# Kernel tuning notes

Hardware: AMD Instinct MI355X
Metric: run time of the kernel (lower is better)

Reference implementation:

```python
import jax, jax.numpy as jnp
import numpy as np

N = 50000      # nodes
E = 800000     # edges (before self-loops)
F_IN = 128     # input node features
H = 4          # attention heads
C = 32         # hidden channels per head (concat width = H*C = 128)
CLS = 40       # num classes (layer 4, concat=False -> mean over heads)
NEG_SLOPE = 0.2


def setup_inputs() -> dict:
    key = jax.random.key(0)
    ks = jax.random.split(key, 16)
    w = lambda k, shape: (jax.random.normal(k, shape, jnp.float32) * 0.1)
    return {
        "x": jax.random.normal(ks[0], (N, F_IN), jnp.float32),
        "edge_index": jax.random.randint(ks[1], (2, E), 0, N),
        "W1": w(ks[2], (F_IN, H * C)), "att_src1": w(ks[3], (H, C)), "att_dst1": w(ks[4], (H, C)), "b1": jnp.zeros((H * C,), jnp.float32),
        "W2": w(ks[5], (H * C, H * C)), "att_src2": w(ks[6], (H, C)), "att_dst2": w(ks[7], (H, C)), "b2": jnp.zeros((H * C,), jnp.float32),
        "W3": w(ks[8], (H * C, H * C)), "att_src3": w(ks[9], (H, C)), "att_dst3": w(ks[10], (H, C)), "b3": jnp.zeros((H * C,), jnp.float32),
        "W4": w(ks[11], (H * C, H * CLS)), "att_src4": w(ks[12], (H, CLS)), "att_dst4": w(ks[13], (H, CLS)), "b4": jnp.zeros((CLS,), jnp.float32),
    }


def _gat(x, W, a_src, a_dst, b, src, dst, n, heads, ch, concat):
    # Linear transform, per-head view: [n, heads, ch]
    h = (x @ W).reshape(n, heads, ch)
    # per-node scalar attention terms [n, heads]
    es = (h * a_src).sum(-1)
    ed = (h * a_dst).sum(-1)
    # edge logits: alpha_j (source) + alpha_i (target), leaky relu (PyG GATConv)
    e = jax.nn.leaky_relu(es[src] + ed[dst], NEG_SLOPE)  # [Etot, heads]
    # segment softmax over incoming edges of each dst node (self-loops guarantee >=1 edge)
    m = jax.ops.segment_max(e, dst, num_segments=n)
    ealpha = jnp.exp(e - m[dst])
    denom = jax.ops.segment_sum(ealpha, dst, num_segments=n)
    alpha = ealpha / denom[dst]
    # weighted message aggregation (scatter-add)
    out = jax.ops.segment_sum(h[src] * alpha[:, :, None], dst, num_segments=n)
    out = out.reshape(n, heads * ch) if concat else out.mean(axis=1)
    return out + b


def reference(x, edge_index, W1, att_src1, att_dst1, b1, W2, att_src2, att_dst2, b2,
              W3, att_src3, att_dst3, b3, W4, att_src4, att_dst4, b4):
    n = x.shape[0]
    loop = jnp.arange(n)
    src = jnp.concatenate([edge_index[0], loop])  # add self-loops (PyG default)
    dst = jnp.concatenate([edge_index[1], loop])
    # dropout layers are identity in eval mode (training=False)
    h = _gat(x, W1, att_src1, att_dst1, b1, src, dst, n, H, C, True)
    h = jax.nn.relu(h)
    h = _gat(h, W2, att_src2, att_dst2, b2, src, dst, n, H, C, True)
    h = jax.nn.relu(h)
    h = _gat(h, W3, att_src3, att_dst3, b3, src, dst, n, H, C, True)
    h = jax.nn.relu(h)
    h = _gat(h, W4, att_src4, att_dst4, b4, src, dst, n, H, CLS, False)
    return h
```

## Files before the change

### kernel.cpp

```cpp
#include <hip/hip_runtime.h>
#include <math.h>

#define NN 50000
#define EE 800000
#define ET (EE + NN)
#define NCHK ((NN + 255) / 256)
#define NEG 0.2f

__device__ __forceinline__ float lrelu(float x) { return x > 0.f ? x : NEG * x; }

typedef __bf16 bf16x8 __attribute__((ext_vector_type(8)));
typedef float f32x4 __attribute__((ext_vector_type(4)));


__global__ __launch_bounds__(256) void k_hist(const int* __restrict__ eidx, int* __restrict__ cnt) {
    int i = blockIdx.x * 256 + threadIdx.x;
    if (i < EE) atomicAdd(&cnt[eidx[EE + i]], 1);
}

__global__ __launch_bounds__(256) void k_csum(const int* __restrict__ cnt, int* __restrict__ csums) {
    __shared__ int sh[256];
    int t = threadIdx.x, i = blockIdx.x * 256 + t;
    sh[t] = (i < NN) ? cnt[i] + 1 : 0;
    __syncthreads();
    for (int off = 128; off > 0; off >>= 1) {
        if (t < off) sh[t] += sh[t + off];
        __syncthreads();
    }
    if (t == 0) csums[blockIdx.x] = sh[0];
}

__global__ __launch_bounds__(256) void k_chscan(const int* __restrict__ cnt, const int* __restrict__ csums,
                                                int* __restrict__ rowptr, int* __restrict__ cursor) {
    __shared__ int sh[256];
    __shared__ int shc[256];
    int t = threadIdx.x, b = blockIdx.x, i = b * 256 + t;
    int v = (i < NN) ? cnt[i] + 1 : 0;
    sh[t] = v;
    shc[t] = (t < NCHK) ? csums[t] : 0;
    __syncthreads();
    for (int off = 1; off < 256; off <<= 1) {
        int x1 = (t >= off) ? sh[t - off] : 0;
        int x2 = (t >= off) ? shc[t - off] : 0;
        __syncthreads();
        sh[t] += x1;
        shc[t] += x2;
        __syncthreads();
    }
    int cbase = (b == 0) ? 0 : shc[b - 1];
    int ex = (t == 0 ? 0 : sh[t - 1]) + cbase;
    if (i < NN) { rowptr[i] = ex; cursor[i] = ex; }
    if (b == 0 && t == 0) rowptr[NN] = ET;
}

__global__ __launch_bounds__(256) void k_scatter(const int* __restrict__ eidx,
                                                 int* __restrict__ cursor, int* __restrict__ ssrc) {
    int i = blockIdx.x * 256 + threadIdx.x;
    if (i >= ET) return;
    int s, d;
    if (i < EE) { s = eidx[i]; d = eidx[EE + i]; } else { s = d = i - EE; }
    int pos = atomicAdd(&cursor[d], 1);
    ssrc[pos] = s;
}


__global__ __launch_bounds__(256) void k_wsplit_all(const float* __restrict__ W0, const float* __restrict__ W1,
                                                    const float* __restrict__ W2, const float* __restrict__ W3,
                                                    __bf16* __restrict__ wsp) {
    int i = blockIdx.x * 256 + threadIdx.x;
    const float* Wm; int NOUT, j; size_t base, sz;
    if (i < 16384)      { Wm = W0; NOUT = 128; j = i;          base = 0;     sz = 16384; }
    else if (i < 32768) { Wm = W1; NOUT = 128; j = i - 16384;  base = 32768; sz = 16384; }
    else if (i < 49152) { Wm = W2; NOUT = 128; j = i - 32768;  base = 65536; sz = 16384; }
    else if (i < 69632) { Wm = W3; NOUT = 160; j = i - 49152;  base = 98304; sz = 20480; }
    else return;
    float v = Wm[j];
    int k = j / NOUT, c = j - k * NOUT;
    __bf16 hi = (__bf16)v;
    __bf16 lo = (__bf16)(v - (float)hi);
    size_t off = base + ((size_t)(k >> 3) * NOUT + c) * 8 + (k & 7);
    wsp[off] = hi;
    wsp[off + sz] = lo;
}


template <int NOUT, bool FUSE>
__global__ __launch_bounds__(256) void k_gemm3(const float* __restrict__ X,
                                               const __bf16* __restrict__ Whi,
                                               const __bf16* __restrict__ Wlo,
                                               float* __restrict__ Y,
                                               const float* __restrict__ asrc,
                                               const float* __restrict__ adst,
                                               float* __restrict__ es, float* __restrict__ ed) {
    constexpr int NT = NOUT / 16;
    constexpr int CH = NOUT / 4;
    int tid = threadIdx.x;
    int w = tid >> 6, l = tid & 63;
    int col = l & 15, kg = l >> 4;
    int rb = blockIdx.x * 128 + w * 32;
    int r0 = rb + col, r1 = rb + 16 + col;
    int rc0 = r0 < NN ? r0 : NN - 1;
    int rc1 = r1 < NN ? r1 : NN - 1;

    f32x4 acc0[NT], acc1[NT];
    #pragma unroll
    for (int t = 0; t < NT; ++t) { acc0[t] = (f32x4){0,0,0,0}; acc1[t] = (f32x4){0,0,0,0}; }

    #pragma unroll
    for (int c4 = 0; c4 < 4; ++c4) {
        bf16x8 ah0, al0, ah1, al1;
        {
            float4 aA = *reinterpret_cast<const float4*>(&X[(size_t)rc0 * 128 + c4 * 32 + kg * 8]);
            float4 aB = *reinterpret_cast<const float4*>(&X[(size_t)rc0 * 128 + c4 * 32 + kg * 8 + 4]);
            float av[8] = {aA.x, aA.y, aA.z, aA.w, aB.x, aB.y, aB.z, aB.w};
            #pragma unroll
            for (int j = 0; j < 8; ++j) { __bf16 h = (__bf16)av[j]; ah0[j] = h; al0[j] = (__bf16)(av[j] - (float)h); }
        }
        {
            float4 aA = *reinterpret_cast<const float4*>(&X[(size_t)rc1 * 128 + c4 * 32 + kg * 8]);
            float4 aB = *reinterpret_cast<const float4*>(&X[(size_t)rc1 * 128 + c4 * 32 + kg * 8 + 4]);
            float av[8] = {aA.x, aA.y, aA.z, aA.w, aB.x, aB.y, aB.z, aB.w};
            #pragma unroll
            for (int j = 0; j < 8; ++j) { __bf16 h = (__bf16)av[j]; ah1[j] = h; al1[j] = (__bf16)(av[j] - (float)h); }
        }
        const __bf16* bh = Whi + ((size_t)(c4 * 4 + kg) * NOUT) * 8;
        const __bf16* bl = Wlo + ((size_t)(c4 * 4 + kg) * NOUT) * 8;
        #pragma unroll
        for (int t = 0; t < NT; ++t) {
            bf16x8 bhi = *reinterpret_cast<const bf16x8*>(bh + (t * 16 + col) * 8);
            bf16x8 blo = *reinterpret_cast<const bf16x8*>(bl + (t * 16 + col) * 8);
            acc0[t] = __builtin_amdgcn_mfma_f32_16x16x32_bf16(ah0, bhi, acc0[t], 0, 0, 0);
            acc0[t] = __builtin_amdgcn_mfma_f32_16x16x32_bf16(al0, bhi, acc0[t], 0, 0, 0);
            acc0[t] = __builtin_amdgcn_mfma_f32_16x16x32_bf16(ah0, blo, acc0[t], 0, 0, 0);
            acc1[t] = __builtin_amdgcn_mfma_f32_16x16x32_bf16(ah1, bhi, acc1[t], 0, 0, 0);
            acc1[t] = __builtin_amdgcn_mfma_f32_16x16x32_bf16(al1, bhi, acc1[t], 0, 0, 0);
            acc1[t] = __builtin_amdgcn_mfma_f32_16x16x32_bf16(ah1, blo, acc1[t], 0, 0, 0);
        }
    }

    #pragma unroll
    for (int t = 0; t < NT; ++t) {
        int cc = t * 16 + col;
        #pragma unroll
        for (int i = 0; i < 4; ++i) {
            int ra = rb + kg * 4 + i;
            int rbq = rb + 16 + kg * 4 + i;
            if (ra < NN)  Y[(size_t)ra  * NOUT + cc] = acc0[t][i];
            if (rbq < NN) Y[(size_t)rbq * NOUT + cc] = acc1[t][i];
        }
    }

    if constexpr (FUSE) {
        float pes[2][4][4], ped[2][4][4];
        #pragma unroll
        for (int rt = 0; rt < 2; ++rt)
            #pragma unroll
            for (int h = 0; h < 4; ++h)
                #pragma unroll
                for (int i = 0; i < 4; ++i) { pes[rt][h][i] = 0.f; ped[rt][h][i] = 0.f; }
        #pragma unroll
        for (int t = 0; t < NT; ++t) {
            float as = asrc[t * 16 + col];
            float ad = adst[t * 16 + col];
            int hA = (t * 16) / CH;
            int hB = (t * 16 + 15) / CH;
            if (hA == hB) {
                #pragma unroll
                for (int i = 0; i < 4; ++i) {
                    pes[0][hA][i] += acc0[t][i] * as;  ped[0][hA][i] += acc0[t][i] * ad;
                    pes[1][hA][i] += acc1[t][i] * as;  ped[1][hA][i] += acc1[t][i] * ad;
                }
            } else {
                bool isB = (col >= (hB * CH - t * 16));
                #pragma unroll
                for (int i = 0; i < 4; ++i) {
                    float vs0 = acc0[t][i] * as, vd0 = acc0[t][i] * ad;
                    float vs1 = acc1[t][i] * as, vd1 = acc1[t][i] * ad;
                    pes[0][hA][i] += isB ? 0.f : vs0;  pes[0][hB][i] += isB ? vs0 : 0.f;
                    ped[0][hA][i] += isB ? 0.f : vd0;  ped[0][hB][i] += isB ? vd0 : 0.f;
                    pes[1][hA][i] += isB ? 0.f : vs1;  pes[1][hB][i] += isB ? vs1 : 0.f;
                    ped[1][hA][i] += isB ? 0.f : vd1;  ped[1][hB][i] += isB ? vd1 : 0.f;
                }
            }
        }
        #pragma unroll
        for (int off = 1; off < 16; off <<= 1) {
            #pragma unroll
            for (int rt = 0; rt < 2; ++rt)
                #pragma unroll
                for (int h = 0; h < 4; ++h)
                    #pragma unroll
                    for (int i = 0; i < 4; ++i) {
                        pes[rt][h][i] += __shfl_xor(pes[rt][h][i], off);
                        ped[rt][h][i] += __shfl_xor(ped[rt][h][i], off);
                    }
        }
        if (col == 0) {
            #pragma unroll
            for (int rt = 0; rt < 2; ++rt)
                #pragma unroll
                for (int i = 0; i < 4; ++i) {
                    int rr = rb + rt * 16 + kg * 4 + i;
                    if (rr < NN) {
                        #pragma unroll
                        for (int h = 0; h < 4; ++h) {
                            es[rr * 4 + h] = pes[rt][h][i];
                            ed[rr * 4 + h] = ped[rt][h][i];
                        }
                    }
                }
        }
    }
}


__global__ __launch_bounds__(256) void k_agg128(const float* __restrict__ Hf,
                                                const float* __restrict__ es, const float* __restrict__ ed,
                                                const int* __restrict__ rowptr, const int* __restrict__ ssrc,
                                                const float* __restrict__ bias, float* __restrict__ Yout) {
    int wid = (blockIdx.x * 256 + threadIdx.x) >> 6;
    int lane = threadIdx.x & 63;
    if (wid >= NN) return;
    int n = wid;
    int beg = rowptr[n], end = rowptr[n + 1];
    int h1 = lane & 3;
    int eoff = lane >> 2;
    float edv = ed[n * 4 + h1];

    float m = -1e30f, dsum = 0.f;
    for (int idx = beg + eoff; idx < end; idx += 16) {
        int s = ssrc[idx];
        float e = lrelu(es[s * 4 + h1] + edv);
        float M = fmaxf(m, e);
        dsum = dsum * __expf(m - M) + __expf(e - M);
        m = M;
    }
    #pragma unroll
    for (int off = 4; off < 64; off <<= 1) {
        float om = __shfl_xor(m, off);
        float od = __shfl_xor(dsum, off);
        float M = fmaxf(m, om);
        dsum = dsum * __expf(m - M) + od * __expf(om - M);
        m = M;
    }
    float invd = 1.f / dsum;

    int q = lane & 7;
    int eg8 = lane >> 3;
    f32x4 acc4[4];
    #pragma unroll
    for (int i = 0; i < 4; ++i) acc4[i] = (f32x4){0.f, 0.f, 0.f, 0.f};

    int nch = (end - beg + 15) >> 4;
    int base = beg;
    for (int ch = 0; ch < nch; ++ch, base += 16) {
        int myIdx = base + eoff;
        int s = ssrc[myIdx < end ? myIdx : end - 1];
        float e = lrelu(es[s * 4 + h1] + edv);
        float alpha = (myIdx < end) ? __expf(e - m) * invd : 0.f;
        #pragma unroll
        for (int hb = 0; hb < 2; ++hb) {
            int e16 = hb * 8 + eg8;
            int se = __shfl(s, e16 * 4);
            const float* rowp = Hf + (size_t)se * 128 + q * 4;
            #pragma unroll
            for (int i = 0; i < 4; ++i) {
                float p = __shfl(alpha, e16 * 4 + i);
                float4 v = *reinterpret_cast<const float4*>(rowp + i * 32);
                acc4[i].x += p * v.x;
                acc4[i].y += p * v.y;
                acc4[i].z += p * v.z;
                acc4[i].w += p * v.w;
            }
        }
    }

    #pragma unroll
    for (int off = 8; off < 64; off <<= 1) {
        #pragma unroll
        for (int i = 0; i < 4; ++i) {
            acc4[i].x += __shfl_xor(acc4[i].x, off);
            acc4[i].y += __shfl_xor(acc4[i].y, off);
            acc4[i].z += __shfl_xor(acc4[i].z, off);
            acc4[i].w += __shfl_xor(acc4[i].w, off);
        }
    }
    if (lane < 8) {
        #pragma unroll
        for (int i = 0; i < 4; ++i) {
            int c0 = 32 * i + 4 * lane;
            float4 bv = *reinterpret_cast<const float4*>(&bias[c0]);
            float4 o;
            o.x = fmaxf(acc4[i].x + bv.x, 0.f);
            o.y = fmaxf(acc4[i].y + bv.y, 0.f);
            o.z = fmaxf(acc4[i].z + bv.z, 0.f);
            o.w = fmaxf(acc4[i].w + bv.w, 0.f);
            *reinterpret_cast<float4*>(&Yout[(size_t)n * 128 + c0]) = o;
        }
    }
}


__global__ __launch_bounds__(256) void k_agg160_mean(const float* __restrict__ Hf,
                                                     const float* __restrict__ es, const float* __restrict__ ed,
                                                     const int* __restrict__ rowptr, const int* __restrict__ ssrc,
                                                     const float* __restrict__ b4, float* __restrict__ out) {
    __shared__ float buf[4][160];
    int wid = (blockIdx.x * 256 + threadIdx.x) >> 6;
    int lane = threadIdx.x & 63;
    int w = threadIdx.x >> 6;
    if (wid >= NN) return;
    int n = wid;
    int beg = rowptr[n], end = rowptr[n + 1];
    int h1 = lane & 3;
    int eoff = lane >> 2;
    float edv = ed[n * 4 + h1];

    float m = -1e30f, dsum = 0.f;
    for (int idx = beg + eoff; idx < end; idx += 16) {
        int s = ssrc[idx];
        float e = lrelu(es[s * 4 + h1] + edv);
        float M = fmaxf(m, e);
        dsum = dsum * __expf(m - M) + __expf(e - M);
        m = M;
    }
    #pragma unroll
    for (int off = 4; off < 64; off <<= 1) {
        float om = __shfl_xor(m, off);
        float od = __shfl_xor(dsum, off);
        float M = fmaxf(m, om);
        dsum = dsum * __expf(m - M) + od * __expf(om - M);
        m = M;
    }
    float invd = 1.f / dsum;

    int q = lane & 7;
    int eg8 = lane >> 3;
    int hh[5];
    #pragma unroll
    for (int i = 0; i < 5; ++i) hh[i] = (i * 8 + q) / 10;
    f32x4 acc4[5];
    #pragma unroll
    for (int i = 0; i < 5; ++i) acc4[i] = (f32x4){0.f, 0.f, 0.f, 0.f};

    int nch = (end - beg + 15) >> 4;
    int base = beg;
    for (int ch = 0; ch < nch; ++ch, base += 16) {
        int myIdx = base + eoff;
        int s = ssrc[myIdx < end ? myIdx : end - 1];
        float e = lrelu(es[s * 4 + h1] + edv);
        float alpha = (myIdx < end) ? __expf(e - m) * invd : 0.f;
        #pragma unroll
        for (int hb = 0; hb < 2; ++hb) {
            int e16 = hb * 8 + eg8;
            int se = __shfl(s, e16 * 4);
            const float* rowp = Hf + (size_t)se * 160 + q * 4;
            #pragma unroll
            for (int i = 0; i < 5; ++i) {
                float p = __shfl(alpha, e16 * 4 + hh[i]);
                float4 v = *reinterpret_cast<const float4*>(rowp + i * 32);
                acc4[i].x += p * v.x;
                acc4[i].y += p * v.y;
                acc4[i].z += p * v.z;
                acc4[i].w += p * v.w;
            }
        }
    }

    #pragma unroll
    for (int off = 8; off < 64; off <<= 1) {
        #pragma unroll
        for (int i = 0; i < 5; ++i) {
            acc4[i].x += __shfl_xor(acc4[i].x, off);
            acc4[i].y += __shfl_xor(acc4[i].y, off);
            acc4[i].z += __shfl_xor(acc4[i].z, off);
            acc4[i].w += __shfl_xor(acc4[i].w, off);
        }
    }
    if (lane < 8) {
        #pragma unroll
        for (int i = 0; i < 5; ++i)
            *reinterpret_cast<float4*>(&buf[w][32 * i + 4 * lane]) = (float4){acc4[i].x, acc4[i].y, acc4[i].z, acc4[i].w};
    }
    __builtin_amdgcn_wave_barrier();
    if (lane < 40) {
        float v = 0.25f * (buf[w][lane] + buf[w][lane + 40] + buf[w][lane + 80] + buf[w][lane + 120]) + b4[lane];
        out[(size_t)n * 40 + lane] = v;
    }
}


extern "C" void kernel_launch(void* const* d_in, const int* in_sizes, int n_in,
                              void* d_out, int out_size, void* d_ws, size_t ws_size,
                              hipStream_t stream) {
    const float* x    = (const float*)d_in[0];
    const int*   eidx = (const int*)d_in[1];
    const float* W[4]    = {(const float*)d_in[2], (const float*)d_in[6], (const float*)d_in[10], (const float*)d_in[14]};
    const float* asrc[4] = {(const float*)d_in[3], (const float*)d_in[7], (const float*)d_in[11], (const float*)d_in[15]};
    const float* adst[4] = {(const float*)d_in[4], (const float*)d_in[8], (const float*)d_in[12], (const float*)d_in[16]};
    const float* bias[4] = {(const float*)d_in[5], (const float*)d_in[9], (const float*)d_in[13], (const float*)d_in[17]};
    float* out = (float*)d_out;

    float* hA = (float*)d_ws;
    float* hB = hA + (size_t)NN * 160;
    float* es = hB + (size_t)NN * 160;
    float* ed = es + (size_t)NN * 4;
    int* rowptr = (int*)(ed + (size_t)NN * 4);
    int* cnt    = rowptr + (NN + 1);
    int* cursor = cnt + NN;
    int* ssrc   = cursor + NN;
    int* csums  = ssrc + ET;
    __bf16* wsp = (__bf16*)(csums + 256);
    __bf16* Whi[4], *Wlo[4];
    {
        __bf16* p = wsp;
        for (int i = 0; i < 4; ++i) {
            int sz = 128 * (i == 3 ? 160 : 128);
            Whi[i] = p; p += sz;
            Wlo[i] = p; p += sz;
        }
    }

    hipMemsetAsync(cnt, 0, NN * sizeof(int), stream);
    k_hist<<<(EE + 255) / 256, 256, 0, stream>>>(eidx, cnt);
    k_csum<<<NCHK, 256, 0, stream>>>(cnt, csums);
    k_chscan<<<NCHK, 256, 0, stream>>>(cnt, csums, rowptr, cursor);
    k_scatter<<<(ET + 255) / 256, 256, 0, stream>>>(eidx, cursor, ssrc);

    k_wsplit_all<<<(69632 + 255) / 256, 256, 0, stream>>>(W[0], W[1], W[2], W[3], wsp);

    int gemmBlocks = (NN + 127) / 128;
    int aggBlocks = (NN * 64 + 255) / 256;

    k_gemm3<128, true><<<gemmBlocks, 256, 0, stream>>>(x, Whi[0], Wlo[0], hA, asrc[0], adst[0], es, ed);
    k_agg128<<<aggBlocks, 256, 0, stream>>>(hA, es, ed, rowptr, ssrc, bias[0], hB);

    k_gemm3<128, true><<<gemmBlocks, 256, 0, stream>>>(hB, Whi[1], Wlo[1], hA, asrc[1], adst[1], es, ed);
    k_agg128<<<aggBlocks, 256, 0, stream>>>(hA, es, ed, rowptr, ssrc, bias[1], hB);

    k_gemm3<128, true><<<gemmBlocks, 256, 0, stream>>>(hB, Whi[2], Wlo[2], hA, asrc[2], adst[2], es, ed);
    k_agg128<<<aggBlocks, 256, 0, stream>>>(hA, es, ed, rowptr, ssrc, bias[2], hB);

    k_gemm3<160, true><<<gemmBlocks, 256, 0, stream>>>(hB, Whi[3], Wlo[3], hA, asrc[3], adst[3], es, ed);
    k_agg160_mean<<<aggBlocks, 256, 0, stream>>>(hA, es, ed, rowptr, ssrc, bias[3], out);
}
```

Baseline: 473.8 us.

## Fold attention vectors into weights and use single-pass unnormalized softmax aggregation

Precomputes W·a_src and W·a_dst per head as extra padded output columns, so the GEMM produces the attention scalars es/ed directly through MFMA and the shuffle-reduction epilogue goes away. The aggregation kernels drop the separate online max/sum pass and instead accumulate exp(e) unnormalized in one pass, dividing by the summed denominator at the end. They also prefetch the next edge's source index and es value. Skipping the max subtraction risks exp overflow if logits get large.

```diff
diff --git a/kernel.cpp b/kernel.cpp
--- a/kernel.cpp
+++ b/kernel.cpp
@@ -64,36 +64,51 @@
 }
 
 
-__global__ __launch_bounds__(256) void k_wsplit_all(const float* __restrict__ W0, const float* __restrict__ W1,
-                                                    const float* __restrict__ W2, const float* __restrict__ W3,
-                                                    __bf16* __restrict__ wsp) {
+__global__ __launch_bounds__(256) void k_wsplit2(const float* __restrict__ W0, const float* __restrict__ W1,
+                                                 const float* __restrict__ W2, const float* __restrict__ W3,
+                                                 const float* __restrict__ as0, const float* __restrict__ as1,
+                                                 const float* __restrict__ as2, const float* __restrict__ as3,
+                                                 const float* __restrict__ ad0, const float* __restrict__ ad1,
+                                                 const float* __restrict__ ad2, const float* __restrict__ ad3,
+                                                 __bf16* __restrict__ wsp) {
     int i = blockIdx.x * 256 + threadIdx.x;
-    const float* Wm; int NOUT, j; size_t base, sz;
-    if (i < 16384)      { Wm = W0; NOUT = 128; j = i;          base = 0;     sz = 16384; }
-    else if (i < 32768) { Wm = W1; NOUT = 128; j = i - 16384;  base = 32768; sz = 16384; }
-    else if (i < 49152) { Wm = W2; NOUT = 128; j = i - 32768;  base = 65536; sz = 16384; }
-    else if (i < 69632) { Wm = W3; NOUT = 160; j = i - 49152;  base = 98304; sz = 20480; }
+    const float *Wm, *asv, *adv; int NOUT, CH, j; size_t base, sz;
+    if (i < 18432)      { Wm = W0; asv = as0; adv = ad0; NOUT = 128; CH = 32; j = i;          base = 0;      sz = 18432; }
+    else if (i < 36864) { Wm = W1; asv = as1; adv = ad1; NOUT = 128; CH = 32; j = i - 18432;  base = 36864;  sz = 18432; }
+    else if (i < 55296) { Wm = W2; asv = as2; adv = ad2; NOUT = 128; CH = 32; j = i - 36864;  base = 73728;  sz = 18432; }
+    else if (i < 77824) { Wm = W3; asv = as3; adv = ad3; NOUT = 160; CH = 40; j = i - 55296;  base = 110592; sz = 22528; }
     else return;
-    float v = Wm[j];
-    int k = j / NOUT, c = j - k * NOUT;
+    int NOUTP = NOUT + 16;
+    int k = j / NOUTP, c = j - k * NOUTP;
+    float v;
+    if (c < NOUT) {
+        v = Wm[k * NOUT + c];
+    } else if (c < NOUT + 8) {
+        int h = (c - NOUT) & 3;
+        const float* av = (c < NOUT + 4) ? asv : adv;
+        float sacc = 0.f;
+        for (int cc = 0; cc < CH; ++cc) sacc += Wm[k * NOUT + h * CH + cc] * av[h * CH + cc];
+        v = sacc;
+    } else {
+        v = 0.f;
+    }
     __bf16 hi = (__bf16)v;
     __bf16 lo = (__bf16)(v - (float)hi);
-    size_t off = base + ((size_t)(k >> 3) * NOUT + c) * 8 + (k & 7);
+    size_t off = base + ((size_t)(k >> 3) * NOUTP + c) * 8 + (k & 7);
     wsp[off] = hi;
     wsp[off + sz] = lo;
 }
 
 
-template <int NOUT, bool FUSE>
-__global__ __launch_bounds__(256) void k_gemm3(const float* __restrict__ X,
+template <int NOUT>
+__global__ __launch_bounds__(256) void k_gemm4(const float* __restrict__ X,
                                                const __bf16* __restrict__ Whi,
                                                const __bf16* __restrict__ Wlo,
                                                float* __restrict__ Y,
-                                               const float* __restrict__ asrc,
-                                               const float* __restrict__ adst,
                                                float* __restrict__ es, float* __restrict__ ed) {
     constexpr int NT = NOUT / 16;
-    constexpr int CH = NOUT / 4;
+    constexpr int NTP = NT + 1;
+    constexpr int NOUTP = NOUT + 16;
     int tid = threadIdx.x;
     int w = tid >> 6, l = tid & 63;
     int col = l & 15, kg = l >> 4;
@@ -102,9 +117,9 @@
     int rc0 = r0 < NN ? r0 : NN - 1;
     int rc1 = r1 < NN ? r1 : NN - 1;
 
-    f32x4 acc0[NT], acc1[NT];
-    #pragma unroll
-    for (int t = 0; t < NT; ++t) { acc0[t] = (f32x4){0,0,0,0}; acc1[t] = (f32x4){0,0,0,0}; }
+    f32x4 acc0[NTP], acc1[NTP];
+    #pragma unroll
+    for (int t = 0; t < NTP; ++t) { acc0[t] = (f32x4){0,0,0,0}; acc1[t] = (f32x4){0,0,0,0}; }
 
     #pragma unroll
     for (int c4 = 0; c4 < 4; ++c4) {
@@ -123,10 +138,10 @@
             #pragma unroll
             for (int j = 0; j < 8; ++j) { __bf16 h = (__bf16)av[j]; ah1[j] = h; al1[j] = (__bf16)(av[j] - (float)h); }
         }
-        const __bf16* bh = Whi + ((size_t)(c4 * 4 + kg) * NOUT) * 8;
-        const __bf16* bl = Wlo + ((size_t)(c4 * 4 + kg) * NOUT) * 8;
-        #pragma unroll
-        for (int t = 0; t < NT; ++t) {
+        const __bf16* bh = Whi + ((size_t)(c4 * 4 + kg) * NOUTP) * 8;
+        const __bf16* bl = Wlo + ((size_t)(c4 * 4 + kg) * NOUTP) * 8;
+        #pragma unroll
+        for (int t = 0; t < NTP; ++t) {
             bf16x8 bhi = *reinterpret_cast<const bf16x8*>(bh + (t * 16 + col) * 8);
             bf16x8 blo = *reinterpret_cast<const bf16x8*>(bl + (t * 16 + col) * 8);
             acc0[t] = __builtin_amdgcn_mfma_f32_16x16x32_bf16(ah0, bhi, acc0[t], 0, 0, 0);
@@ -149,66 +164,16 @@
             if (rbq < NN) Y[(size_t)rbq * NOUT + cc] = acc1[t][i];
         }
     }
-
-    if constexpr (FUSE) {
-        float pes[2][4][4], ped[2][4][4];
-        #pragma unroll
-        for (int rt = 0; rt < 2; ++rt)
-            #pragma unroll
-            for (int h = 0; h < 4; ++h)
-                #pragma unroll
-                for (int i = 0; i < 4; ++i) { pes[rt][h][i] = 0.f; ped[rt][h][i] = 0.f; }
-        #pragma unroll
-        for (int t = 0; t < NT; ++t) {
-            float as = asrc[t * 16 + col];
-            float ad = adst[t * 16 + col];
-            int hA = (t * 16) / CH;
-            int hB = (t * 16 + 15) / CH;
-            if (hA == hB) {
-                #pragma unroll
-                for (int i = 0; i < 4; ++i) {
-                    pes[0][hA][i] += acc0[t][i] * as;  ped[0][hA][i] += acc0[t][i] * ad;
-                    pes[1][hA][i] += acc1[t][i] * as;  ped[1][hA][i] += acc1[t][i] * ad;
-                }
-            } else {
-                bool isB = (col >= (hB * CH - t * 16));
-                #pragma unroll
-                for (int i = 0; i < 4; ++i) {
-                    float vs0 = acc0[t][i] * as, vd0 = acc0[t][i] * ad;
-                    float vs1 = acc1[t][i] * as, vd1 = acc1[t][i] * ad;
-                    pes[0][hA][i] += isB ? 0.f : vs0;  pes[0][hB][i] += isB ? vs0 : 0.f;
-                    ped[0][hA][i] += isB ? 0.f : vd0;  ped[0][hB][i] += isB ? vd0 : 0.f;
-                    pes[1][hA][i] += isB ? 0.f : vs1;  pes[1][hB][i] += isB ? vs1 : 0.f;
-                    ped[1][hA][i] += isB ? 0.f : vd1;  ped[1][hB][i] += isB ? vd1 : 0.f;
-                }
-            }
-        }
-        #pragma unroll
-        for (int off = 1; off < 16; off <<= 1) {
-            #pragma unroll
-            for (int rt = 0; rt < 2; ++rt)
-                #pragma unroll
-                for (int h = 0; h < 4; ++h)
-                    #pragma unroll
-                    for (int i = 0; i < 4; ++i) {
-                        pes[rt][h][i] += __shfl_xor(pes[rt][h][i], off);
-                        ped[rt][h][i] += __shfl_xor(ped[rt][h][i], off);
-                    }
-        }
-        if (col == 0) {
-            #pragma unroll
-            for (int rt = 0; rt < 2; ++rt)
-                #pragma unroll
-                for (int i = 0; i < 4; ++i) {
-                    int rr = rb + rt * 16 + kg * 4 + i;
-                    if (rr < NN) {
-                        #pragma unroll
-                        for (int h = 0; h < 4; ++h) {
-                            es[rr * 4 + h] = pes[rt][h][i];
-                            ed[rr * 4 + h] = ped[rt][h][i];
-                        }
-                    }
-                }
+    #pragma unroll
+    for (int i = 0; i < 4; ++i) {
+        int ra = rb + kg * 4 + i;
+        int rbq = rb + 16 + kg * 4 + i;
+        if (col < 4) {
+            if (ra < NN)  es[ra * 4 + col] = acc0[NT][i];
+            if (rbq < NN) es[rbq * 4 + col] = acc1[NT][i];
+        } else if (col < 8) {
+            if (ra < NN)  ed[ra * 4 + col - 4] = acc0[NT][i];
+            if (rbq < NN) ed[rbq * 4 + col - 4] = acc1[NT][i];
         }
     }
 }
@@ -226,54 +191,49 @@
     int h1 = lane & 3;
     int eoff = lane >> 2;
     float edv = ed[n * 4 + h1];
-
-    float m = -1e30f, dsum = 0.f;
-    for (int idx = beg + eoff; idx < end; idx += 16) {
-        int s = ssrc[idx];
-        float e = lrelu(es[s * 4 + h1] + edv);
-        float M = fmaxf(m, e);
-        dsum = dsum * __expf(m - M) + __expf(e - M);
-        m = M;
-    }
-    #pragma unroll
-    for (int off = 4; off < 64; off <<= 1) {
-        float om = __shfl_xor(m, off);
-        float od = __shfl_xor(dsum, off);
-        float M = fmaxf(m, om);
-        dsum = dsum * __expf(m - M) + od * __expf(om - M);
-        m = M;
-    }
-    float invd = 1.f / dsum;
-
     int q = lane & 7;
     int eg8 = lane >> 3;
+
     f32x4 acc4[4];
     #pragma unroll
     for (int i = 0; i < 4; ++i) acc4[i] = (f32x4){0.f, 0.f, 0.f, 0.f};
+    float dsum = 0.f;
 
     int nch = (end - beg + 15) >> 4;
-    int base = beg;
-    for (int ch = 0; ch < nch; ++ch, base += 16) {
-        int myIdx = base + eoff;
-        int s = ssrc[myIdx < end ? myIdx : end - 1];
-        float e = lrelu(es[s * 4 + h1] + edv);
-        float alpha = (myIdx < end) ? __expf(e - m) * invd : 0.f;
+    int myIdx = beg + eoff;
+    int s_cur = ssrc[myIdx < end ? myIdx : end - 1];
+    float esv = es[s_cur * 4 + h1];
+    for (int ch = 0; ch < nch; ++ch) {
+        int nIdx = myIdx + 16;
+        int s_nxt = ssrc[nIdx < end ? nIdx : end - 1];
+        float e = lrelu(esv + edv);
+        float p = (myIdx < end) ? __expf(e) : 0.f;
+        dsum += p;
         #pragma unroll
         for (int hb = 0; hb < 2; ++hb) {
             int e16 = hb * 8 + eg8;
-            int se = __shfl(s, e16 * 4);
+            int se = __shfl(s_cur, e16 * 4);
             const float* rowp = Hf + (size_t)se * 128 + q * 4;
             #pragma unroll
             for (int i = 0; i < 4; ++i) {
-                float p = __shfl(alpha, e16 * 4 + i);
+                float pp = __shfl(p, e16 * 4 + i);
                 float4 v = *reinterpret_cast<const float4*>(rowp + i * 32);
-                acc4[i].x += p * v.x;
-                acc4[i].y += p * v.y;
-                acc4[i].z += p * v.z;
-                acc4[i].w += p * v.w;
+                acc4[i].x += pp * v.x;
+                acc4[i].y += pp * v.y;
+                acc4[i].z += pp * v.z;
+                acc4[i].w += pp * v.w;
             }
         }
-    }
+        float esv_n = es[s_nxt * 4 + h1];
+        s_cur = s_nxt; esv = esv_n; myIdx = nIdx;
+    }
+
+    #pragma unroll
+    for (int off = 4; off < 64; off <<= 1) dsum += __shfl_xor(dsum, off);
+    float inv0 = 1.f / __shfl(dsum, 0);
+    float inv1 = 1.f / __shfl(dsum, 1);
+    float inv2 = 1.f / __shfl(dsum, 2);
+    float inv3 = 1.f / __shfl(dsum, 3);
 
     #pragma unroll
     for (int off = 8; off < 64; off <<= 1) {
@@ -286,15 +246,16 @@
         }
     }
     if (lane < 8) {
+        float inv[4] = {inv0, inv1, inv2, inv3};
         #pragma unroll
         for (int i = 0; i < 4; ++i) {
             int c0 = 32 * i + 4 * lane;
             float4 bv = *reinterpret_cast<const float4*>(&bias[c0]);
             float4 o;
-            o.x = fmaxf(acc4[i].x + bv.x, 0.f);
-            o.y = fmaxf(acc4[i].y + bv.y, 0.f);
-            o.z = fmaxf(acc4[i].z + bv.z, 0.f);
-            o.w = fmaxf(acc4[i].w + bv.w, 0.f);
+            o.x = fmaxf(acc4[i].x * inv[i] + bv.x, 0.f);
+            o.y = fmaxf(acc4[i].y * inv[i] + bv.y, 0.f);
+            o.z = fmaxf(acc4[i].z * inv[i] + bv.z, 0.f);
+            o.w = fmaxf(acc4[i].w * inv[i] + bv.w, 0.f);
             *reinterpret_cast<float4*>(&Yout[(size_t)n * 128 + c0]) = o;
         }
     }
@@ -306,6 +267,7 @@
                                                      const int* __restrict__ rowptr, const int* __restrict__ ssrc,
                                                      const float* __restrict__ b4, float* __restrict__ out) {
     __shared__ float buf[4][160];
+    __shared__ float bufd[4][4];
     int wid = (blockIdx.x * 256 + threadIdx.x) >> 6;
     int lane = threadIdx.x & 63;
     int w = threadIdx.x >> 6;
@@ -315,57 +277,48 @@
     int h1 = lane & 3;
     int eoff = lane >> 2;
     float edv = ed[n * 4 + h1];
-
-    float m = -1e30f, dsum = 0.f;
-    for (int idx = beg + eoff; idx < end; idx += 16) {
-        int s = ssrc[idx];
-        float e = lrelu(es[s * 4 + h1] + edv);
-        float M = fmaxf(m, e);
-        dsum = dsum * __expf(m - M) + __expf(e - M);
-        m = M;
-    }
-    #pragma unroll
-    for (int off = 4; off < 64; off <<= 1) {
-        float om = __shfl_xor(m, off);
-        float od = __shfl_xor(dsum, off);
-        float M = fmaxf(m, om);
-        dsum = dsum * __expf(m - M) + od * __expf(om - M);
-        m = M;
-    }
-    float invd = 1.f / dsum;
-
     int q = lane & 7;
     int eg8 = lane >> 3;
     int hh[5];
     #pragma unroll
     for (int i = 0; i < 5; ++i) hh[i] = (i * 8 + q) / 10;
+
     f32x4 acc4[5];
     #pragma unroll
     for (int i = 0; i < 5; ++i) acc4[i] = (f32x4){0.f, 0.f, 0.f, 0.f};
+    float dsum = 0.f;
 
     int nch = (end - beg + 15) >> 4;
-    int base = beg;
-    for (int ch = 0; ch < nch; ++ch, base += 16) {
-        int myIdx = base + eoff;
-        int s = ssrc[myIdx < end ? myIdx : end - 1];
-        float e = lrelu(es[s * 4 + h1] + edv);
-        float alpha = (myIdx < end) ? __expf(e - m) * invd : 0.f;
+    int myIdx = beg + eoff;
+    int s_cur = ssrc[myIdx < end ? myIdx : end - 1];
+    float esv = es[s_cur * 4 + h1];
+    for (int ch = 0; ch < nch; ++ch) {
+        int nIdx = myIdx + 16;
+        int s_nxt = ssrc[nIdx < end ? nIdx : end - 1];
+        float e = lrelu(esv + edv);
+        float p = (myIdx < end) ? __expf(e) : 0.f;
+        dsum += p;
         #pragma unroll
         for (int hb = 0; hb < 2; ++hb) {
             int e16 = hb * 8 + eg8;
-            int se = __shfl(s, e16 * 4);
+            int se = __shfl(s_cur, e16 * 4);
             const float* rowp = Hf + (size_t)se * 160 + q * 4;
             #pragma unroll
             for (int i = 0; i < 5; ++i) {
-                float p = __shfl(alpha, e16 * 4 + hh[i]);
+                float pp = __shfl(p, e16 * 4 + hh[i]);
                 float4 v = *reinterpret_cast<const float4*>(rowp + i * 32);
-                acc4[i].x += p * v.x;
-                acc4[i].y += p * v.y;
-                acc4[i].z += p * v.z;
-                acc4[i].w += p * v.w;
+                acc4[i].x += pp * v.x;
+                acc4[i].y += pp * v.y;
+                acc4[i].z += pp * v.z;
+                acc4[i].w += pp * v.w;
             }
         }
-    }
+        float esv_n = es[s_nxt * 4 + h1];
+        s_cur = s_nxt; esv = esv_n; myIdx = nIdx;
+    }
+
+    #pragma unroll
+    for (int off = 4; off < 64; off <<= 1) dsum += __shfl_xor(dsum, off);
 
     #pragma unroll
     for (int off = 8; off < 64; off <<= 1) {
@@ -382,9 +335,13 @@
         for (int i = 0; i < 5; ++i)
             *reinterpret_cast<float4*>(&buf[w][32 * i + 4 * lane]) = (float4){acc4[i].x, acc4[i].y, acc4[i].z, acc4[i].w};
     }
+    if (lane < 4) bufd[w][lane] = 1.f / dsum;
     __builtin_amdgcn_wave_barrier();
     if (lane < 40) {
-        float v = 0.25f * (buf[w][lane] + buf[w][lane + 40] + buf[w][lane + 80] + buf[w][lane + 120]) + b4[lane];
+        float v = 0.25f * (buf[w][lane]       * bufd[w][0] +
+                           buf[w][lane + 40]  * bufd[w][1] +
+                           buf[w][lane + 80]  * bufd[w][2] +
+                           buf[w][lane + 120] * bufd[w][3]) + b4[lane];
         out[(size_t)n * 40 + lane] = v;
     }
 }
@@ -411,15 +368,8 @@
     int* ssrc   = cursor + NN;
     int* csums  = ssrc + ET;
     __bf16* wsp = (__bf16*)(csums + 256);
-    __bf16* Whi[4], *Wlo[4];
-    {
-        __bf16* p = wsp;
-        for (int i = 0; i < 4; ++i) {
-            int sz = 128 * (i == 3 ? 160 : 128);
-            Whi[i] = p; p += sz;
-            Wlo[i] = p; p += sz;
-        }
-    }
+    __bf16* Whi[4] = {wsp, wsp + 36864, wsp + 73728, wsp + 110592};
+    __bf16* Wlo[4] = {wsp + 18432, wsp + 55296, wsp + 92160, wsp + 133120};
 
     hipMemsetAsync(cnt, 0, NN * sizeof(int), stream);
     k_hist<<<(EE + 255) / 256, 256, 0, stream>>>(eidx, cnt);
@@ -427,20 +377,22 @@
     k_chscan<<<NCHK, 256, 0, stream>>>(cnt, csums, rowptr, cursor);
     k_scatter<<<(ET + 255) / 256, 256, 0, stream>>>(eidx, cursor, ssrc);
 
-    k_wsplit_all<<<(69632 + 255) / 256, 256, 0, stream>>>(W[0], W[1], W[2], W[3], wsp);
+    k_wsplit2<<<(77824 + 255) / 256, 256, 0, stream>>>(W[0], W[1], W[2], W[3],
+                                                       asrc[0], asrc[1], asrc[2], asrc[3],
+                                                       adst[0], adst[1], adst[2], adst[3], wsp);
 
     int gemmBlocks = (NN + 127) / 128;
     int aggBlocks = (NN * 64 + 255) / 256;
 
-    k_gemm3<128, true><<<gemmBlocks, 256, 0, stream>>>(x, Whi[0], Wlo[0], hA, asrc[0], adst[0], es, ed);
+    k_gemm4<128><<<gemmBlocks, 256, 0, stream>>>(x, Whi[0], Wlo[0], hA, es, ed);
     k_agg128<<<aggBlocks, 256, 0, stream>>>(hA, es, ed, rowptr, ssrc, bias[0], hB);
 
-    k_gemm3<128, true><<<gemmBlocks, 256, 0, stream>>>(hB, Whi[1], Wlo[1], hA, asrc[1], adst[1], es, ed);
+    k_gemm4<128><<<gemmBlocks, 256, 0, stream>>>(hB, Whi[1], Wlo[1], hA, es, ed);
     k_agg128<<<aggBlocks, 256, 0, stream>>>(hA, es, ed, rowptr, ssrc, bias[1], hB);
 
-    k_gemm3<128, true><<<gemmBlocks, 256, 0, stream>>>(hB, Whi[2], Wlo[2], hA, asrc[2], adst[2], es, ed);
+    k_gemm4<128><<<gemmBlocks, 256, 0, stream>>>(hB, Whi[2], Wlo[2], hA, es, ed);
     k_agg128<<<aggBlocks, 256, 0, stream>>>(hA, es, ed, rowptr, ssrc, bias[2], hB);
 
-    k_gemm3<160, true><<<gemmBlocks, 256, 0, stream>>>(hB, Whi[3], Wlo[3], hA, asrc[3], adst[3], es, ed);
+    k_gemm4<160><<<gemmBlocks, 256, 0, stream>>>(hB, Whi[3], Wlo[3], hA, es, ed);
     k_agg160_mean<<<aggBlocks, 256, 0, stream>>>(hA, es, ed, rowptr, ssrc, bias[3], out);
 }
```

Result: no change. 465.1 us (-1.8%).
